# Optimization experiments

Measured on AMD Instinct MI355X. Metric: run time of the kernel, lower is better.

## Reference

```python
import jax, jax.numpy as jnp
import numpy as np

TEMP = 16.0  # sqrt(in_dim=256), module default when temperature=None
BN_EPS = 1e-5


def setup_inputs() -> dict:
    key = jax.random.key(0)
    ks = jax.random.split(key, 8)
    B, Cin, T, H, W = 8, 256, 8, 16, 16
    FF, Cout = 512, 256
    # small init scale keeps softmax logits in a sane range
    s = 0.02
    return {
        "x": jax.random.normal(ks[0], (B, Cin, T, H, W), jnp.float32),
        "Wk": jax.random.normal(ks[1], (FF, Cin), jnp.float32) * s,
        "Wq": jax.random.normal(ks[2], (FF, Cin), jnp.float32) * s,
        "Wv": jax.random.normal(ks[3], (FF, Cin), jnp.float32) * s,
        "Wout": jax.random.normal(ks[4], (Cout, FF), jnp.float32) * s,
        "bout": jax.random.normal(ks[5], (Cout,), jnp.float32) * s,
        "gamma": jnp.ones((Cout,), jnp.float32),
        "beta": jnp.zeros((Cout,), jnp.float32),
    }


def reference(x, Wk, Wq, Wv, Wout, bout, gamma, beta):
    B, Cin, T, H, W = x.shape
    N = T * H * W
    xf = x.reshape(B, Cin, N)                      # 1x1x1 conv == per-position matmul
    K = jnp.einsum('fc,bcn->bfn', Wk, xf)
    Q = jnp.einsum('fc,bcn->bfn', Wq, xf)
    V = jnp.einsum('fc,bcn->bfn', Wv, xf)
    KQ = jnp.einsum('bfi,bfj->bij', K, Q)          # [B, N, N] = K^T Q
    attn = jax.nn.softmax(KQ / TEMP, axis=2)
    # torch: sum(V[:, :, :, None] * attn[:, None], dim=3)
    #      = V[b,c,i] * sum_j attn[b,i,j]  (no need to materialize B x C x N x N)
    agg = V * jnp.sum(attn, axis=2)[:, None, :]    # [B, FF, N]
    o = jnp.einsum('of,bfn->bon', Wout, agg) + bout[None, :, None]
    o = jax.nn.relu(o).reshape(B, -1, T, H, W)
    y = x + o                                      # residual (in_dim == out_dim)
    # BatchNorm3d, training mode (fresh module): batch stats over (B, T, H, W)
    mean = jnp.mean(y, axis=(0, 2, 3, 4), keepdims=True)
    var = jnp.var(y, axis=(0, 2, 3, 4), keepdims=True)
    g = gamma[None, :, None, None, None]
    b = beta[None, :, None, None, None]
    return g * (y - mean) * jax.lax.rsqrt(var + BN_EPS) + b
```

## Files before the change

### kernel.cpp

```cpp
#include <hip/hip_runtime.h>

typedef __attribute__((ext_vector_type(8))) short short8;
typedef __attribute__((ext_vector_type(4))) float floatx4;

#define CIN  256
#define NSP  2048
#define COUT 256
#define FF   512
#define NSHARD 32

__device__ unsigned short g_M[COUT * CIN];
__device__ float g_shard[NSHARD][2][COUT];

__device__ __forceinline__ unsigned short f2bf_rne(float f) {
  unsigned int u = __float_as_uint(f);
  u += 0x7fffu + ((u >> 16) & 1u);
  return (unsigned short)(u >> 16);
}

__device__ __forceinline__ unsigned int pack_bf16_hu(float lo, float hi) {
  unsigned int a = __float_as_uint(lo) + 0x8000u;
  unsigned int b = __float_as_uint(hi) + 0x8000u;
  return __builtin_amdgcn_perm(b, a, 0x07060302u);
}

__global__ __launch_bounds__(1024) void k1_m(
    const float* __restrict__ Wv, const float* __restrict__ Wout)
{
  __shared__ float ws[512];
  __shared__ float red[4][256];
  const int tid = threadIdx.x;
  const int r   = blockIdx.x;
  if (r == 0) {
    float* gs = &g_shard[0][0][0];
    #pragma unroll
    for (int i = 0; i < 16; ++i) gs[tid + i * 1024] = 0.f;
  }
  if (tid < 512) ws[tid] = Wout[(size_t)r * 512 + tid];
  __syncthreads();
  const int c  = tid & 255;
  const int fs = tid >> 8;
  float acc = 0.f;
  #pragma unroll 16
  for (int f0 = 0; f0 < 128; ++f0) {
    int f = fs * 128 + f0;
    acc += ws[f] * Wv[(size_t)f * 256 + c];
  }
  red[fs][c] = acc;
  __syncthreads();
  if (tid < 256) {
    float s = red[0][tid] + red[1][tid] + red[2][tid] + red[3][tid];
    g_M[(size_t)r * 256 + tid] = f2bf_rne(s);
  }
}

__global__ __launch_bounds__(256, 2) void k2_gemm(
    const float* __restrict__ x, const float* __restrict__ bout,
    float* __restrict__ out)
{
  __shared__ float ls[128], lq[128];
  const int tid  = threadIdx.x;
  const int lane = tid & 63;
  const int wave = tid >> 6;
  const int m16  = lane & 15;
  const int q    = lane >> 4;
  const int nb   = blockIdx.x * 64;
  const int ocb  = blockIdx.y * 128;
  const int b    = blockIdx.z;
  const int wocb = ocb + (wave & 1) * 64;
  const int wnb  = nb + (wave >> 1) * 32;

  if (tid < 128) { ls[tid] = 0.f; lq[tid] = 0.f; }

  floatx4 acc[4][2];
  #pragma unroll
  for (int i = 0; i < 4; ++i)
    #pragma unroll
    for (int j = 0; j < 2; ++j)
      acc[i][j] = (floatx4){0.f, 0.f, 0.f, 0.f};

  const unsigned short* Ab = g_M + (size_t)(wocb + m16) * 256 + q * 8;
  const float* xb = x + (size_t)b * CIN * NSP;
  const float* Bb = xb + (size_t)(q * 8) * NSP + wnb + m16;

  #pragma unroll
  for (int kk = 0; kk < 8; ++kk) {
    short8 av[4];
    #pragma unroll
    for (int ti = 0; ti < 4; ++ti)
      av[ti] = *(const short8*)(Ab + (size_t)ti * 16 * 256 + kk * 32);
    short8 bv[2];
    #pragma unroll
    for (int tj = 0; tj < 2; ++tj) {
      const float* bp = Bb + (size_t)(kk * 32) * NSP + tj * 16;
      union { unsigned int u[4]; short8 v; } p;
      #pragma unroll
      for (int j = 0; j < 4; ++j) {
        float f0 = bp[(size_t)(2 * j) * NSP];
        float f1 = bp[(size_t)(2 * j + 1) * NSP];
        p.u[j] = pack_bf16_hu(f0, f1);
      }
      bv[tj] = p.v;
    }
    #pragma unroll
    for (int ti = 0; ti < 4; ++ti)
      #pragma unroll
      for (int tj = 0; tj < 2; ++tj)
        acc[ti][tj] = __builtin_amdgcn_mfma_f32_16x16x32_bf16(av[ti], bv[tj], acc[ti][tj], 0, 0, 0);
  }

  __syncthreads();

  #pragma unroll
  for (int ti = 0; ti < 4; ++ti) {
    #pragma unroll
    for (int r = 0; r < 4; ++r) {
      const int ocl = (wave & 1) * 64 + ti * 16 + q * 4 + r;
      const int oc  = ocb + ocl;
      const float bo = bout[oc];
      float s = 0.f, s2 = 0.f;
      #pragma unroll
      for (int tj = 0; tj < 2; ++tj) {
        const int n = wnb + tj * 16 + m16;
        const size_t gidx = ((size_t)(b * COUT + oc)) * NSP + n;
        float o = fmaxf(acc[ti][tj][r] + bo, 0.f);
        float y = x[gidx] + o;
        out[gidx] = y;
        s += y;
        s2 += y * y;
      }
      #pragma unroll
      for (int d = 1; d < 16; d <<= 1) {
        s  += __shfl_xor(s, d, 64);
        s2 += __shfl_xor(s2, d, 64);
      }
      if (m16 == 0) {
        atomicAdd(&ls[ocl], s);
        atomicAdd(&lq[ocl], s2);
      }
    }
  }
  __syncthreads();
  if (tid < 128) {
    const int s = blockIdx.x;
    atomicAdd(&g_shard[s][0][ocb + tid], ls[tid]);
    atomicAdd(&g_shard[s][1][ocb + tid], lq[tid]);
  }
}

__global__ __launch_bounds__(256) void k3_norm(
    const float* __restrict__ gamma, const float* __restrict__ beta,
    float* __restrict__ out)
{
  const int row = blockIdx.x;
  const int oc  = row & 255;
  float su = 0.f, sq = 0.f;
  #pragma unroll
  for (int i = 0; i < NSHARD; ++i) {
    su += g_shard[i][0][oc];
    sq += g_shard[i][1][oc];
  }
  const float inv_n = 1.f / 16384.f;
  const float m  = su * inv_n;
  const float v  = sq * inv_n - m * m;
  const float sc = gamma[oc] * rsqrtf(v + 1e-5f);
  const float sh = beta[oc] - m * sc;
  float* p = out + (size_t)row * 2048 + threadIdx.x * 8;
  float4 a = *(const float4*)p;
  float4 c = *(const float4*)(p + 4);
  a.x = a.x * sc + sh; a.y = a.y * sc + sh;
  a.z = a.z * sc + sh; a.w = a.w * sc + sh;
  c.x = c.x * sc + sh; c.y = c.y * sc + sh;
  c.z = c.z * sc + sh; c.w = c.w * sc + sh;
  *(float4*)p = a;
  *(float4*)(p + 4) = c;
}

extern "C" void kernel_launch(void* const* d_in, const int* in_sizes, int n_in,
                              void* d_out, int out_size, void* d_ws, size_t ws_size,
                              hipStream_t stream) {
  const float* x     = (const float*)d_in[0];
  const float* Wv    = (const float*)d_in[3];
  const float* Wout  = (const float*)d_in[4];
  const float* bout  = (const float*)d_in[5];
  const float* gamma = (const float*)d_in[6];
  const float* beta  = (const float*)d_in[7];
  float* out = (float*)d_out;

  hipLaunchKernelGGL(k1_m,    dim3(256),       dim3(1024), 0, stream,
                     Wv, Wout);
  hipLaunchKernelGGL(k2_gemm, dim3(32, 2, 8),  dim3(256),  0, stream,
                     x, bout, out);
  hipLaunchKernelGGL(k3_norm, dim3(2048),      dim3(256),  0, stream,
                     gamma, beta, out);
}
```

Measured before the change: 116.4 us.

## Stage x tile in LDS and compute all output channels per block

The GEMM kernel now loads a 256x64 slab of x into padded shared memory once per block and covers all 256 output channels with 8 waves, instead of splitting output channels across two blocks that each re-read x from global memory. The residual add also reads x from LDS rather than global memory. This removes redundant global reads of x and the strided per-element global loads in the MFMA loop. In exchange it uses about 66KB of LDS per block, which limits occupancy, and it adds a sync before compute.

```diff
diff --git a/kernel.cpp b/kernel.cpp
--- a/kernel.cpp
+++ b/kernel.cpp
@@ -8,6 +8,7 @@
 #define COUT 256
 #define FF   512
 #define NSHARD 32
+#define LPAD 66
 
 __device__ unsigned short g_M[COUT * CIN];
 __device__ float g_shard[NSHARD][2][COUT];
@@ -54,23 +55,40 @@
   }
 }
 
-__global__ __launch_bounds__(256, 2) void k2_gemm(
+__global__ __launch_bounds__(512, 2) void k2_gemm(
     const float* __restrict__ x, const float* __restrict__ bout,
     float* __restrict__ out)
 {
-  __shared__ float ls[128], lq[128];
+  __shared__ float lx[CIN * LPAD];
+  __shared__ float ls[COUT], lq[COUT];
   const int tid  = threadIdx.x;
   const int lane = tid & 63;
   const int wave = tid >> 6;
   const int m16  = lane & 15;
   const int q    = lane >> 4;
-  const int nb   = blockIdx.x * 64;
-  const int ocb  = blockIdx.y * 128;
-  const int b    = blockIdx.z;
-  const int wocb = ocb + (wave & 1) * 64;
-  const int wnb  = nb + (wave >> 1) * 32;
-
-  if (tid < 128) { ls[tid] = 0.f; lq[tid] = 0.f; }
+  const int id   = blockIdx.x;
+  const int b    = id & 7;
+  const int n0   = (id >> 3) * 64;
+  const int wocb = (wave & 3) * 64;
+  const int wn   = (wave >> 2) * 32;
+
+  if (tid < COUT) { ls[tid] = 0.f; lq[tid] = 0.f; }
+
+  {
+    const int n4 = (tid & 15) * 4;
+    const int cr = tid >> 5;
+    const int ch = (tid >> 4) & 1;
+    const float* gp = x + (size_t)b * CIN * NSP + n0 + n4;
+    #pragma unroll
+    for (int i = 0; i < 8; ++i) {
+      const int c = cr + 16 * (2 * i + ch);
+      const float4 v = *(const float4*)(gp + (size_t)c * NSP);
+      float* d = &lx[c * LPAD + n4];
+      *(float2*)d       = make_float2(v.x, v.y);
+      *(float2*)(d + 2) = make_float2(v.z, v.w);
+    }
+  }
+  __syncthreads();
 
   floatx4 acc[4][2];
   #pragma unroll
@@ -80,8 +98,6 @@
       acc[i][j] = (floatx4){0.f, 0.f, 0.f, 0.f};
 
   const unsigned short* Ab = g_M + (size_t)(wocb + m16) * 256 + q * 8;
-  const float* xb = x + (size_t)b * CIN * NSP;
-  const float* Bb = xb + (size_t)(q * 8) * NSP + wnb + m16;
 
   #pragma unroll
   for (int kk = 0; kk < 8; ++kk) {
@@ -92,12 +108,13 @@
     short8 bv[2];
     #pragma unroll
     for (int tj = 0; tj < 2; ++tj) {
-      const float* bp = Bb + (size_t)(kk * 32) * NSP + tj * 16;
+      const int nl = wn + tj * 16 + m16;
+      const float* lp = &lx[(kk * 32 + q * 8) * LPAD + nl];
       union { unsigned int u[4]; short8 v; } p;
       #pragma unroll
       for (int j = 0; j < 4; ++j) {
-        float f0 = bp[(size_t)(2 * j) * NSP];
-        float f1 = bp[(size_t)(2 * j + 1) * NSP];
+        float f0 = lp[(2 * j) * LPAD];
+        float f1 = lp[(2 * j + 1) * LPAD];
         p.u[j] = pack_bf16_hu(f0, f1);
       }
       bv[tj] = p.v;
@@ -109,22 +126,19 @@
         acc[ti][tj] = __builtin_amdgcn_mfma_f32_16x16x32_bf16(av[ti], bv[tj], acc[ti][tj], 0, 0, 0);
   }
 
-  __syncthreads();
-
   #pragma unroll
   for (int ti = 0; ti < 4; ++ti) {
     #pragma unroll
     for (int r = 0; r < 4; ++r) {
-      const int ocl = (wave & 1) * 64 + ti * 16 + q * 4 + r;
-      const int oc  = ocb + ocl;
+      const int oc = wocb + ti * 16 + q * 4 + r;
       const float bo = bout[oc];
       float s = 0.f, s2 = 0.f;
       #pragma unroll
       for (int tj = 0; tj < 2; ++tj) {
-        const int n = wnb + tj * 16 + m16;
-        const size_t gidx = ((size_t)(b * COUT + oc)) * NSP + n;
+        const int nl = wn + tj * 16 + m16;
+        const size_t gidx = ((size_t)(b * COUT + oc)) * NSP + n0 + nl;
         float o = fmaxf(acc[ti][tj][r] + bo, 0.f);
-        float y = x[gidx] + o;
+        float y = lx[oc * LPAD + nl] + o;
         out[gidx] = y;
         s += y;
         s2 += y * y;
@@ -135,16 +149,16 @@
         s2 += __shfl_xor(s2, d, 64);
       }
       if (m16 == 0) {
-        atomicAdd(&ls[ocl], s);
-        atomicAdd(&lq[ocl], s2);
+        atomicAdd(&ls[oc], s);
+        atomicAdd(&lq[oc], s2);
       }
     }
   }
   __syncthreads();
-  if (tid < 128) {
-    const int s = blockIdx.x;
-    atomicAdd(&g_shard[s][0][ocb + tid], ls[tid]);
-    atomicAdd(&g_shard[s][1][ocb + tid], lq[tid]);
+  if (tid < COUT) {
+    const int s = id >> 3;
+    atomicAdd(&g_shard[s][0][tid], ls[tid]);
+    atomicAdd(&g_shard[s][1][tid], lq[tid]);
   }
 }
 
@@ -187,10 +201,8 @@
   const float* beta  = (const float*)d_in[7];
   float* out = (float*)d_out;
 
-  hipLaunchKernelGGL(k1_m,    dim3(256),       dim3(1024), 0, stream,
-                     Wv, Wout);
-  hipLaunchKernelGGL(k2_gemm, dim3(32, 2, 8),  dim3(256),  0, stream,
-                     x, bout, out);
-  hipLaunchKernelGGL(k3_norm, dim3(2048),      dim3(256),  0, stream,
+  hipLaunchKernelGGL(k1_m,    dim3(256),  dim3(1024), 0, stream, Wv, Wout);
+  hipLaunchKernelGGL(k2_gemm, dim3(256),  dim3(512),  0, stream, x, bout, out);
+  hipLaunchKernelGGL(k3_norm, dim3(2048), dim3(256),  0, stream,
                      gamma, beta, out);
 }
```

After: 112.9 us, median of 2. 1.03x faster.
